# Kernel tuning notes

Measured on AMD Instinct MI355X. Metric: run time of the kernel, lower is better.

Reference implementation:

```python
import jax, jax.numpy as jnp
import numpy as np

N = 100000
IN_C = 128
OUT_C = 128
E = 1600000


def setup_inputs() -> dict:
    key = jax.random.key(0)
    k1, k2, k3, k4 = jax.random.split(key, 4)
    x = jax.random.normal(k1, (N, IN_C), dtype=jnp.float32)
    edge_index = jax.random.randint(k2, (2, E), 0, N, dtype=jnp.int64)
    # GCNConv params: linear weight (stored [in, out] for x @ W) and bias [out]
    W = jax.random.normal(k3, (IN_C, OUT_C), dtype=jnp.float32) / np.sqrt(IN_C)
    b = jax.random.normal(k4, (OUT_C,), dtype=jnp.float32) * 0.01
    return {"x": x, "edge_index": edge_index, "W": W, "b": b}


def reference(x, edge_index, W, b):
    n = x.shape[0]
    # add self loops (PyG GCNConv default add_self_loops=True)
    loop = jnp.arange(n, dtype=edge_index.dtype)
    src = jnp.concatenate([edge_index[0], loop])  # message sources
    dst = jnp.concatenate([edge_index[1], loop])  # aggregation targets
    # symmetric normalization: deg over targets (edge weight 1, incl. self loops)
    deg = jax.ops.segment_sum(jnp.ones_like(dst, dtype=x.dtype), dst, num_segments=n)
    dinv = jnp.where(deg > 0, jax.lax.rsqrt(deg), 0.0)
    norm = dinv[src] * dinv[dst]  # [E+N]
    # linear transform then gather-scale-scatter aggregation
    h = x @ W  # [N, out]
    msgs = h[src] * norm[:, None]  # [E+N, out] -- dominant memory traffic
    out = jax.ops.segment_sum(msgs, dst, num_segments=n)
    return out + b
```

## Files before the change

kernel.cpp:

```cpp
#include <hip/hip_runtime.h>


#define SCAN_T 256
#define SCAN_E 1024
#define WPB 4
#define CAP 1536
#define SC_T 4096

typedef __attribute__((ext_vector_type(8))) short short8;
typedef __attribute__((ext_vector_type(4))) float f32x4;

__device__ __forceinline__ unsigned short f2bf(float f) {
  unsigned int u = __float_as_uint(f);
  u += 0x7FFFu + ((u >> 16) & 1u);
  return (unsigned short)(u >> 16);
}
__device__ __forceinline__ float bf_lo(unsigned int u) { return __uint_as_float(u << 16); }
__device__ __forceinline__ float bf_hi(unsigned int u) { return __uint_as_float(u & 0xFFFF0000u); }


__global__ void k_zero(int* __restrict__ p, int m) {
  int i = blockIdx.x * blockDim.x + threadIdx.x;
  if (i < m) p[i] = 0;
}

__global__ void __launch_bounds__(256) k_scatter(
    const int* __restrict__ ei, int* __restrict__ bcursor,
    int* __restrict__ pairs, int E, int B) {
  __shared__ int hist[2048];
  int t = threadIdx.x;
  for (int b = t; b < B; b += 256) hist[b] = 0;
  __syncthreads();
  int e0 = blockIdx.x * SC_T;
  int eend = min(e0 + SC_T, E);
  for (int e = e0 + t * 4; e < eend; e += 1024) {
    if (e + 3 < eend) {
      int4 d = *(const int4*)(ei + E + e);
      atomicAdd(&hist[((unsigned)d.x) >> 6], 1);
      atomicAdd(&hist[((unsigned)d.y) >> 6], 1);
      atomicAdd(&hist[((unsigned)d.z) >> 6], 1);
      atomicAdd(&hist[((unsigned)d.w) >> 6], 1);
    } else {
      for (int q = e; q < eend; ++q) atomicAdd(&hist[((unsigned)ei[E + q]) >> 6], 1);
    }
  }
  __syncthreads();
  for (int b = t; b < B; b += 256) {
    int c = hist[b];
    hist[b] = c ? atomicAdd(&bcursor[b], c) : 0;
  }
  __syncthreads();
  for (int e = e0 + t * 4; e < eend; e += 1024) {
    if (e + 3 < eend) {
      int4 s = *(const int4*)(ei + e);
      int4 d = *(const int4*)(ei + E + e);
      int b0 = ((unsigned)d.x) >> 6; int p0 = atomicAdd(&hist[b0], 1);
      if (p0 < CAP) pairs[(size_t)b0 * CAP + p0] = ((d.x & 63) << 17) | s.x;
      int b1 = ((unsigned)d.y) >> 6; int p1 = atomicAdd(&hist[b1], 1);
      if (p1 < CAP) pairs[(size_t)b1 * CAP + p1] = ((d.y & 63) << 17) | s.y;
      int b2 = ((unsigned)d.z) >> 6; int p2 = atomicAdd(&hist[b2], 1);
      if (p2 < CAP) pairs[(size_t)b2 * CAP + p2] = ((d.z & 63) << 17) | s.z;
      int b3 = ((unsigned)d.w) >> 6; int p3 = atomicAdd(&hist[b3], 1);
      if (p3 < CAP) pairs[(size_t)b3 * CAP + p3] = ((d.w & 63) << 17) | s.w;
    } else {
      for (int q = e; q < eend; ++q) {
        int dst = ei[E + q], src = ei[q];
        int b0 = ((unsigned)dst) >> 6; int p0 = atomicAdd(&hist[b0], 1);
        if (p0 < CAP) pairs[(size_t)b0 * CAP + p0] = ((dst & 63) << 17) | src;
      }
    }
  }
}

__global__ void __launch_bounds__(256) k_bucket_csr(
    int* __restrict__ pairs, const int* __restrict__ bcursor,
    int* __restrict__ onc, float* __restrict__ dinv, int n) {
  __shared__ int pb[CAP];
  __shared__ int sorted[CAP];
  __shared__ int hist[64], base_[64], cur[64];
  int t = threadIdx.x;
  int b = blockIdx.x;
  int cnt = min(bcursor[b], CAP);
  int* gp = pairs + (size_t)b * CAP;
  for (int i = t; i < cnt; i += 256) pb[i] = gp[i];
  if (t < 64) { hist[t] = 0; cur[t] = 0; }
  __syncthreads();
  for (int i = t; i < cnt; i += 256) atomicAdd(&hist[pb[i] >> 17], 1);
  __syncthreads();
  if (t < 64) {
    int v = hist[t];
    int incl = v;
#pragma unroll
    for (int d = 1; d < 64; d <<= 1) {
      int u = __shfl_up(incl, d, 64);
      if (t >= d) incl += u;
    }
    base_[t] = incl - v;
    int node = b * 64 + t;
    if (node < n) {
      onc[node] = ((incl - v) << 16) | v;
      dinv[node] = rsqrtf((float)v + 1.0f);
    }
  }
  __syncthreads();
  for (int i = t; i < cnt; i += 256) {
    int p = pb[i];
    int d = p >> 17;
    int pos = base_[d] + atomicAdd(&cur[d], 1);
    sorted[pos] = p & 0x1FFFF;
  }
  __syncthreads();
  for (int i = t; i < cnt; i += 256) gp[i] = sorted[i];
}

__global__ void __launch_bounds__(256) k_gemm_h(
    const float* __restrict__ x, const float* __restrict__ W,
    const float* __restrict__ dinv, unsigned short* __restrict__ h, int n) {
  __shared__ alignas(16) unsigned short Wt[128][136];
  int t = threadIdx.x;
#pragma unroll
  for (int p = 0; p < 16; ++p) {
    int task = p * 256 + t;
    int kg = task >> 7, nn = task & 127;
    float w0 = W[(kg * 4 + 0) * 128 + nn];
    float w1 = W[(kg * 4 + 1) * 128 + nn];
    float w2 = W[(kg * 4 + 2) * 128 + nn];
    float w3 = W[(kg * 4 + 3) * 128 + nn];
    ushort4 u;
    u.x = f2bf(w0); u.y = f2bf(w1); u.z = f2bf(w2); u.w = f2bf(w3);
    *(ushort4*)&Wt[nn][kg * 4] = u;
  }
  __syncthreads();
  int w = t >> 6, lane = t & 63;
  int q = lane >> 4, m = lane & 15;
  int r0 = blockIdx.x * 64 + w * 16;
  f32x4 acc[8];
#pragma unroll
  for (int nt = 0; nt < 8; ++nt) acc[nt] = (f32x4){0.f, 0.f, 0.f, 0.f};
  float dscale[4];
#pragma unroll
  for (int rg = 0; rg < 4; ++rg) {
    int r = r0 + q * 4 + rg;
    dscale[rg] = dinv[r < n ? r : n - 1];
  }
#pragma unroll
  for (int ks = 0; ks < 4; ++ks) {
    int row = r0 + m;
    row = row < n ? row : n - 1;
    const float* xp = x + (size_t)row * 128 + ks * 32 + q * 8;
    float4 a0 = *(const float4*)xp;
    float4 a1 = *(const float4*)(xp + 4);
    short8 af;
    af[0] = (short)f2bf(a0.x); af[1] = (short)f2bf(a0.y);
    af[2] = (short)f2bf(a0.z); af[3] = (short)f2bf(a0.w);
    af[4] = (short)f2bf(a1.x); af[5] = (short)f2bf(a1.y);
    af[6] = (short)f2bf(a1.z); af[7] = (short)f2bf(a1.w);
#pragma unroll
    for (int nt = 0; nt < 8; ++nt) {
      short8 bf = *(const short8*)&Wt[nt * 16 + m][ks * 32 + q * 8];
      acc[nt] = __builtin_amdgcn_mfma_f32_16x16x32_bf16(af, bf, acc[nt], 0, 0, 0);
    }
  }
#pragma unroll
  for (int nt = 0; nt < 8; ++nt)
#pragma unroll
    for (int rg = 0; rg < 4; ++rg) {
      int r = r0 + q * 4 + rg;
      if (r < n) h[(size_t)r * 128 + nt * 16 + m] = f2bf(acc[nt][rg] * dscale[rg]);
    }
}

__global__ void __launch_bounds__(256) k_agg_bias(
    const unsigned int* __restrict__ h2, const float* __restrict__ dinv,
    const int* __restrict__ onc, const int* __restrict__ pairs,
    const float* __restrict__ bias, float* __restrict__ out, int n) {
  int node = blockIdx.x * WPB + (threadIdx.x >> 6);
  int lane = threadIdx.x & 63;
  if (node >= n) return;
  unsigned int sp = h2[(size_t)node * 64 + lane];
  float ax = bf_lo(sp), ay = bf_hi(sp);
  int v = onc[node];
  int s = (node >> 6) * CAP + (v >> 16);
  int end = s + (v & 0xFFFF);
  const int* __restrict__ csr = pairs;
  for (; s + 8 <= end; s += 8) {
    int i0 = csr[s + 0], i1 = csr[s + 1], i2 = csr[s + 2], i3 = csr[s + 3];
    int i4 = csr[s + 4], i5 = csr[s + 5], i6 = csr[s + 6], i7 = csr[s + 7];
    unsigned int u0 = h2[(size_t)i0 * 64 + lane];
    unsigned int u1 = h2[(size_t)i1 * 64 + lane];
    unsigned int u2 = h2[(size_t)i2 * 64 + lane];
    unsigned int u3 = h2[(size_t)i3 * 64 + lane];
    unsigned int u4 = h2[(size_t)i4 * 64 + lane];
    unsigned int u5 = h2[(size_t)i5 * 64 + lane];
    unsigned int u6 = h2[(size_t)i6 * 64 + lane];
    unsigned int u7 = h2[(size_t)i7 * 64 + lane];
    ax += (bf_lo(u0) + bf_lo(u1)) + (bf_lo(u2) + bf_lo(u3)) +
          (bf_lo(u4) + bf_lo(u5)) + (bf_lo(u6) + bf_lo(u7));
    ay += (bf_hi(u0) + bf_hi(u1)) + (bf_hi(u2) + bf_hi(u3)) +
          (bf_hi(u4) + bf_hi(u5)) + (bf_hi(u6) + bf_hi(u7));
  }
  for (; s < end; ++s) {
    unsigned int u = h2[(size_t)csr[s] * 64 + lane];
    ax += bf_lo(u); ay += bf_hi(u);
  }
  float di = dinv[node];
  float2 bb = ((const float2*)bias)[lane];
  float2 r;
  r.x = fmaf(ax, di, bb.x);
  r.y = fmaf(ay, di, bb.y);
  ((float2*)out)[(size_t)node * 64 + lane] = r;
}


__global__ void k_init(int* __restrict__ cnt, int n) {
  int i = blockIdx.x * blockDim.x + threadIdx.x;
  if (i < n) cnt[i] = 0;
}

__global__ void k_count4(const int* __restrict__ ei, int* __restrict__ cnt, int E) {
  int i = blockIdx.x * blockDim.x + threadIdx.x;
  int e = i * 4;
  if (e + 3 < E) {
    int4 d = *(const int4*)(ei + E + e);
    atomicAdd(&cnt[d.x], 1); atomicAdd(&cnt[d.y], 1);
    atomicAdd(&cnt[d.z], 1); atomicAdd(&cnt[d.w], 1);
  } else {
    for (; e < E; ++e) atomicAdd(&cnt[ei[E + e]], 1);
  }
}

__global__ void k_scan_local(const int* __restrict__ cnt, int* __restrict__ offs,
                             int* __restrict__ bsums, int n) {
  __shared__ int sh[SCAN_T];
  int t = threadIdx.x;
  int base = blockIdx.x * SCAN_E + t * 4;
  int v0 = 0, v1 = 0, v2 = 0, v3 = 0;
  if (base + 0 < n) v0 = cnt[base + 0];
  if (base + 1 < n) v1 = cnt[base + 1];
  if (base + 2 < n) v2 = cnt[base + 2];
  if (base + 3 < n) v3 = cnt[base + 3];
  int sum = v0 + v1 + v2 + v3;
  sh[t] = sum;
  __syncthreads();
  for (int d = 1; d < SCAN_T; d <<= 1) {
    int xv = (t >= d) ? sh[t - d] : 0;
    __syncthreads();
    sh[t] += xv;
    __syncthreads();
  }
  int run = sh[t] - sum;
  if (base + 0 < n) offs[base + 0] = run; run += v0;
  if (base + 1 < n) offs[base + 1] = run; run += v1;
  if (base + 2 < n) offs[base + 2] = run; run += v2;
  if (base + 3 < n) offs[base + 3] = run;
  if (t == SCAN_T - 1) bsums[blockIdx.x] = sh[t];
}

__global__ void k_scan_bsums(int* __restrict__ bsums, int nb) {
  __shared__ int sh[SCAN_T];
  int t = threadIdx.x;
  int v = (t < nb) ? bsums[t] : 0;
  sh[t] = v;
  __syncthreads();
  for (int d = 1; d < SCAN_T; d <<= 1) {
    int xv = (t >= d) ? sh[t - d] : 0;
    __syncthreads();
    sh[t] += xv;
    __syncthreads();
  }
  if (t < nb) bsums[t] = sh[t] - v;
}

__global__ void k_scan_finish(int* __restrict__ offs, const int* __restrict__ bsums,
                              const int* __restrict__ cnt, int* __restrict__ offs2,
                              float* __restrict__ dinv, int n) {
  int i = blockIdx.x * blockDim.x + threadIdx.x;
  if (i < n) {
    int o = offs[i] + bsums[i / SCAN_E];
    offs[i] = o;
    offs2[i] = o;
    dinv[i] = rsqrtf((float)cnt[i] + 1.0f);
  }
}

__global__ void k_fill4(const int* __restrict__ ei, int* __restrict__ offs2,
                        int* __restrict__ csr, int E) {
  int i = blockIdx.x * blockDim.x + threadIdx.x;
  int e = i * 4;
  if (e + 3 < E) {
    int4 s = *(const int4*)(ei + e);
    int4 d = *(const int4*)(ei + E + e);
    csr[atomicAdd(&offs2[d.x], 1)] = s.x;
    csr[atomicAdd(&offs2[d.y], 1)] = s.y;
    csr[atomicAdd(&offs2[d.z], 1)] = s.z;
    csr[atomicAdd(&offs2[d.w], 1)] = s.w;
  } else {
    for (; e < E; ++e) csr[atomicAdd(&offs2[ei[E + e]], 1)] = ei[e];
  }
}

__global__ void __launch_bounds__(256) k_agg_bias_csr(
    const unsigned int* __restrict__ h2, const float* __restrict__ dinv,
    const int* __restrict__ offs, const int* __restrict__ cnt,
    const int* __restrict__ csr, const float* __restrict__ bias,
    float* __restrict__ out, int n) {
  int node = blockIdx.x * WPB + (threadIdx.x >> 6);
  int lane = threadIdx.x & 63;
  if (node >= n) return;
  unsigned int sp = h2[(size_t)node * 64 + lane];
  float ax = bf_lo(sp), ay = bf_hi(sp);
  int s = offs[node];
  int end = s + cnt[node];
  for (; s + 8 <= end; s += 8) {
    int i0 = csr[s + 0], i1 = csr[s + 1], i2 = csr[s + 2], i3 = csr[s + 3];
    int i4 = csr[s + 4], i5 = csr[s + 5], i6 = csr[s + 6], i7 = csr[s + 7];
    unsigned int u0 = h2[(size_t)i0 * 64 + lane];
    unsigned int u1 = h2[(size_t)i1 * 64 + lane];
    unsigned int u2 = h2[(size_t)i2 * 64 + lane];
    unsigned int u3 = h2[(size_t)i3 * 64 + lane];
    unsigned int u4 = h2[(size_t)i4 * 64 + lane];
    unsigned int u5 = h2[(size_t)i5 * 64 + lane];
    unsigned int u6 = h2[(size_t)i6 * 64 + lane];
    unsigned int u7 = h2[(size_t)i7 * 64 + lane];
    ax += (bf_lo(u0) + bf_lo(u1)) + (bf_lo(u2) + bf_lo(u3)) +
          (bf_lo(u4) + bf_lo(u5)) + (bf_lo(u6) + bf_lo(u7));
    ay += (bf_hi(u0) + bf_hi(u1)) + (bf_hi(u2) + bf_hi(u3)) +
          (bf_hi(u4) + bf_hi(u5)) + (bf_hi(u6) + bf_hi(u7));
  }
  for (; s < end; ++s) {
    unsigned int u = h2[(size_t)csr[s] * 64 + lane];
    ax += bf_lo(u); ay += bf_hi(u);
  }
  float di = dinv[node];
  float2 bb = ((const float2*)bias)[lane];
  float2 r;
  r.x = fmaf(ax, di, bb.x);
  r.y = fmaf(ay, di, bb.y);
  ((float2*)out)[(size_t)node * 64 + lane] = r;
}

extern "C" void kernel_launch(void* const* d_in, const int* in_sizes, int n_in,
                              void* d_out, int out_size, void* d_ws, size_t ws_size,
                              hipStream_t stream) {
  const float* x = (const float*)d_in[0];
  const int* ei = (const int*)d_in[1];
  const float* Wm = (const float*)d_in[2];
  const float* bias = (const float*)d_in[3];
  float* out = (float*)d_out;

  int N = in_sizes[0] / 128;
  int E = in_sizes[1] / 2;
  int NB = (N + 63) >> 6;

  size_t need_new = (size_t)N * 8 + 8192 + (size_t)NB * CAP * 4 + (size_t)N * 256;

  if (ws_size >= need_new && N <= (1 << 17) && NB <= 2048) {
    char* p = (char*)d_ws;
    float* dinv = (float*)p;       p += (size_t)N * 4;
    int* onc = (int*)p;            p += (size_t)N * 4;
    int* bcursor = (int*)p;        p += 8192;
    int* pairs = (int*)p;          p += (size_t)NB * CAP * 4;
    unsigned short* h = (unsigned short*)p;

    k_zero<<<(NB + 255) / 256, 256, 0, stream>>>(bcursor, NB);
    k_scatter<<<(E + SC_T - 1) / SC_T, 256, 0, stream>>>(ei, bcursor, pairs, E, NB);
    k_bucket_csr<<<NB, 256, 0, stream>>>(pairs, bcursor, onc, dinv, N);
    k_gemm_h<<<NB, 256, 0, stream>>>(x, Wm, dinv, h, N);
    k_agg_bias<<<(N + WPB - 1) / WPB, 256, 0, stream>>>(
        (const unsigned int*)h, dinv, onc, pairs, bias, out, N);
    return;
  }

  char* p = (char*)d_ws;
  int* cnt = (int*)p;        p += (size_t)N * 4;
  int* offs = (int*)p;       p += (size_t)N * 4;
  int* offs2 = (int*)p;      p += (size_t)N * 4;
  float* dinv = (float*)p;   p += (size_t)N * 4;
  int* bsums = (int*)p;      p += 1024;
  int* csr = (int*)p;        p += (size_t)E * 4;
  unsigned short* h = (unsigned short*)p;

  int nb_n = (N + 255) / 256;
  int nb_e4 = ((E + 3) / 4 + 255) / 256;
  int nb_scan = (N + SCAN_E - 1) / SCAN_E;

  k_init<<<nb_n, 256, 0, stream>>>(cnt, N);
  k_count4<<<nb_e4, 256, 0, stream>>>(ei, cnt, E);
  k_scan_local<<<nb_scan, SCAN_T, 0, stream>>>(cnt, offs, bsums, N);
  k_scan_bsums<<<1, SCAN_T, 0, stream>>>(bsums, nb_scan);
  k_scan_finish<<<nb_n, 256, 0, stream>>>(offs, bsums, cnt, offs2, dinv, N);
  k_fill4<<<nb_e4, 256, 0, stream>>>(ei, offs2, csr, E);
  k_gemm_h<<<(N + 63) / 64, 256, 0, stream>>>(x, Wm, dinv, h, N);
  k_agg_bias_csr<<<(N + WPB - 1) / WPB, 256, 0, stream>>>(
      (const unsigned int*)h, dinv, offs, cnt, csr, bias, out, N);
}
```

Measured before the change: 226.7 us.

## Fuse bucket sort with GEMM and enlarge scatter blocks

Merges the per-bucket CSR sort kernel with the dinv-scaled bf16 GEMM into one kernel, so each 64-node block computes the degree normalisation in shared memory and uses it directly in the GEMM epilogue. This removes one launch and the global dinv round-trip between the two stages. The scatter kernel also moves to 512 threads with 8192 edges per block, which halves the number of histogram flushes to global bucket cursors. In exchange the fused kernel uses more shared memory, which may lower occupancy, and the W-to-bf16 staging is now repeated inside every sort block.

```diff
diff --git a/kernel.cpp b/kernel.cpp
--- a/kernel.cpp
+++ b/kernel.cpp
@@ -5,7 +5,7 @@
 #define SCAN_E 1024
 #define WPB 4
 #define CAP 1536
-#define SC_T 4096
+#define SC_T 8192
 
 typedef __attribute__((ext_vector_type(8))) short short8;
 typedef __attribute__((ext_vector_type(4))) float f32x4;
@@ -24,16 +24,16 @@
   if (i < m) p[i] = 0;
 }
 
-__global__ void __launch_bounds__(256) k_scatter(
+__global__ void __launch_bounds__(512) k_scatter(
     const int* __restrict__ ei, int* __restrict__ bcursor,
     int* __restrict__ pairs, int E, int B) {
   __shared__ int hist[2048];
   int t = threadIdx.x;
-  for (int b = t; b < B; b += 256) hist[b] = 0;
+  for (int b = t; b < B; b += 512) hist[b] = 0;
   __syncthreads();
   int e0 = blockIdx.x * SC_T;
   int eend = min(e0 + SC_T, E);
-  for (int e = e0 + t * 4; e < eend; e += 1024) {
+  for (int e = e0 + t * 4; e < eend; e += 2048) {
     if (e + 3 < eend) {
       int4 d = *(const int4*)(ei + E + e);
       atomicAdd(&hist[((unsigned)d.x) >> 6], 1);
@@ -45,12 +45,12 @@
     }
   }
   __syncthreads();
-  for (int b = t; b < B; b += 256) {
+  for (int b = t; b < B; b += 512) {
     int c = hist[b];
     hist[b] = c ? atomicAdd(&bcursor[b], c) : 0;
   }
   __syncthreads();
-  for (int e = e0 + t * 4; e < eend; e += 1024) {
+  for (int e = e0 + t * 4; e < eend; e += 2048) {
     if (e + 3 < eend) {
       int4 s = *(const int4*)(ei + e);
       int4 d = *(const int4*)(ei + E + e);
@@ -72,52 +72,22 @@
   }
 }
 
-__global__ void __launch_bounds__(256) k_bucket_csr(
+__global__ void __launch_bounds__(256) k_sort_gemm(
     int* __restrict__ pairs, const int* __restrict__ bcursor,
-    int* __restrict__ onc, float* __restrict__ dinv, int n) {
+    int* __restrict__ onc, float* __restrict__ dinv,
+    const float* __restrict__ x, const float* __restrict__ W,
+    unsigned short* __restrict__ h, int n) {
+  __shared__ alignas(16) unsigned short Wt[128][136];
   __shared__ int pb[CAP];
   __shared__ int sorted[CAP];
   __shared__ int hist[64], base_[64], cur[64];
+  __shared__ float dloc[64];
   int t = threadIdx.x;
   int b = blockIdx.x;
+  if (t < 64) { hist[t] = 0; cur[t] = 0; }
   int cnt = min(bcursor[b], CAP);
   int* gp = pairs + (size_t)b * CAP;
   for (int i = t; i < cnt; i += 256) pb[i] = gp[i];
-  if (t < 64) { hist[t] = 0; cur[t] = 0; }
-  __syncthreads();
-  for (int i = t; i < cnt; i += 256) atomicAdd(&hist[pb[i] >> 17], 1);
-  __syncthreads();
-  if (t < 64) {
-    int v = hist[t];
-    int incl = v;
-#pragma unroll
-    for (int d = 1; d < 64; d <<= 1) {
-      int u = __shfl_up(incl, d, 64);
-      if (t >= d) incl += u;
-    }
-    base_[t] = incl - v;
-    int node = b * 64 + t;
-    if (node < n) {
-      onc[node] = ((incl - v) << 16) | v;
-      dinv[node] = rsqrtf((float)v + 1.0f);
-    }
-  }
-  __syncthreads();
-  for (int i = t; i < cnt; i += 256) {
-    int p = pb[i];
-    int d = p >> 17;
-    int pos = base_[d] + atomicAdd(&cur[d], 1);
-    sorted[pos] = p & 0x1FFFF;
-  }
-  __syncthreads();
-  for (int i = t; i < cnt; i += 256) gp[i] = sorted[i];
-}
-
-__global__ void __launch_bounds__(256) k_gemm_h(
-    const float* __restrict__ x, const float* __restrict__ W,
-    const float* __restrict__ dinv, unsigned short* __restrict__ h, int n) {
-  __shared__ alignas(16) unsigned short Wt[128][136];
-  int t = threadIdx.x;
 #pragma unroll
   for (int p = 0; p < 16; ++p) {
     int task = p * 256 + t;
@@ -131,18 +101,44 @@
     *(ushort4*)&Wt[nn][kg * 4] = u;
   }
   __syncthreads();
+  for (int i = t; i < cnt; i += 256) atomicAdd(&hist[pb[i] >> 17], 1);
+  __syncthreads();
+  if (t < 64) {
+    int v = hist[t];
+    int incl = v;
+#pragma unroll
+    for (int d = 1; d < 64; d <<= 1) {
+      int u = __shfl_up(incl, d, 64);
+      if (t >= d) incl += u;
+    }
+    base_[t] = incl - v;
+    float di = rsqrtf((float)v + 1.0f);
+    dloc[t] = di;
+    int node = b * 64 + t;
+    if (node < n) {
+      onc[node] = ((incl - v) << 16) | v;
+      dinv[node] = di;
+    }
+  }
+  __syncthreads();
+  for (int i = t; i < cnt; i += 256) {
+    int p = pb[i];
+    int d = p >> 17;
+    int pos = base_[d] + atomicAdd(&cur[d], 1);
+    sorted[pos] = p & 0x1FFFF;
+  }
+  __syncthreads();
+  for (int i = t; i < cnt; i += 256) gp[i] = sorted[i];
+
   int w = t >> 6, lane = t & 63;
   int q = lane >> 4, m = lane & 15;
-  int r0 = blockIdx.x * 64 + w * 16;
+  int r0 = b * 64 + w * 16;
   f32x4 acc[8];
 #pragma unroll
   for (int nt = 0; nt < 8; ++nt) acc[nt] = (f32x4){0.f, 0.f, 0.f, 0.f};
   float dscale[4];
 #pragma unroll
-  for (int rg = 0; rg < 4; ++rg) {
-    int r = r0 + q * 4 + rg;
-    dscale[rg] = dinv[r < n ? r : n - 1];
-  }
+  for (int rg = 0; rg < 4; ++rg) dscale[rg] = dloc[w * 16 + q * 4 + rg];
 #pragma unroll
   for (int ks = 0; ks < 4; ++ks) {
     int row = r0 + m;
@@ -299,6 +295,63 @@
   }
 }
 
+__global__ void __launch_bounds__(256) k_gemm_h(
+    const float* __restrict__ x, const float* __restrict__ W,
+    const float* __restrict__ dinv, unsigned short* __restrict__ h, int n) {
+  __shared__ alignas(16) unsigned short Wt[128][136];
+  int t = threadIdx.x;
+#pragma unroll
+  for (int p = 0; p < 16; ++p) {
+    int task = p * 256 + t;
+    int kg = task >> 7, nn = task & 127;
+    float w0 = W[(kg * 4 + 0) * 128 + nn];
+    float w1 = W[(kg * 4 + 1) * 128 + nn];
+    float w2 = W[(kg * 4 + 2) * 128 + nn];
+    float w3 = W[(kg * 4 + 3) * 128 + nn];
+    ushort4 u;
+    u.x = f2bf(w0); u.y = f2bf(w1); u.z = f2bf(w2); u.w = f2bf(w3);
+    *(ushort4*)&Wt[nn][kg * 4] = u;
+  }
+  __syncthreads();
+  int w = t >> 6, lane = t & 63;
+  int q = lane >> 4, m = lane & 15;
+  int r0 = blockIdx.x * 64 + w * 16;
+  f32x4 acc[8];
+#pragma unroll
+  for (int nt = 0; nt < 8; ++nt) acc[nt] = (f32x4){0.f, 0.f, 0.f, 0.f};
+  float dscale[4];
+#pragma unroll
+  for (int rg = 0; rg < 4; ++rg) {
+    int r = r0 + q * 4 + rg;
+    dscale[rg] = dinv[r < n ? r : n - 1];
+  }
+#pragma unroll
+  for (int ks = 0; ks < 4; ++ks) {
+    int row = r0 + m;
+    row = row < n ? row : n - 1;
+    const float* xp = x + (size_t)row * 128 + ks * 32 + q * 8;
+    float4 a0 = *(const float4*)xp;
+    float4 a1 = *(const float4*)(xp + 4);
+    short8 af;
+    af[0] = (short)f2bf(a0.x); af[1] = (short)f2bf(a0.y);
+    af[2] = (short)f2bf(a0.z); af[3] = (short)f2bf(a0.w);
+    af[4] = (short)f2bf(a1.x); af[5] = (short)f2bf(a1.y);
+    af[6] = (short)f2bf(a1.z); af[7] = (short)f2bf(a1.w);
+#pragma unroll
+    for (int nt = 0; nt < 8; ++nt) {
+      short8 bf = *(const short8*)&Wt[nt * 16 + m][ks * 32 + q * 8];
+      acc[nt] = __builtin_amdgcn_mfma_f32_16x16x32_bf16(af, bf, acc[nt], 0, 0, 0);
+    }
+  }
+#pragma unroll
+  for (int nt = 0; nt < 8; ++nt)
+#pragma unroll
+    for (int rg = 0; rg < 4; ++rg) {
+      int r = r0 + q * 4 + rg;
+      if (r < n) h[(size_t)r * 128 + nt * 16 + m] = f2bf(acc[nt][rg] * dscale[rg]);
+    }
+}
+
 __global__ void __launch_bounds__(256) k_agg_bias_csr(
     const unsigned int* __restrict__ h2, const float* __restrict__ dinv,
     const int* __restrict__ offs, const int* __restrict__ cnt,
@@ -363,9 +416,8 @@
     unsigned short* h = (unsigned short*)p;
 
     k_zero<<<(NB + 255) / 256, 256, 0, stream>>>(bcursor, NB);
-    k_scatter<<<(E + SC_T - 1) / SC_T, 256, 0, stream>>>(ei, bcursor, pairs, E, NB);
-    k_bucket_csr<<<NB, 256, 0, stream>>>(pairs, bcursor, onc, dinv, N);
-    k_gemm_h<<<NB, 256, 0, stream>>>(x, Wm, dinv, h, N);
+    k_scatter<<<(E + SC_T - 1) / SC_T, 512, 0, stream>>>(ei, bcursor, pairs, E, NB);
+    k_sort_gemm<<<NB, 256, 0, stream>>>(pairs, bcursor, onc, dinv, x, Wm, h, N);
     k_agg_bias<<<(N + WPB - 1) / WPB, 256, 0, stream>>>(
         (const unsigned int*)h, dinv, onc, pairs, bias, out, N);
     return;
```

After: 221.2 us. -2.4%, faster.
